# Kernel optimization log

Measured on AMD Instinct MI355X. Metric: run time of the kernel, lower is better.

The kernel has to match this reference:

```python
import jax, jax.numpy as jnp
import numpy as np

FRAME_LENGTH = 800
FRAME_STEP = 200
FFT_LENGTH = 800


def _hann_window(n):
    # tf.signal.hann_window default: periodic=True -> 0.5 - 0.5*cos(2*pi*k/n)
    k = jnp.arange(n, dtype=jnp.float32)
    return 0.5 - 0.5 * jnp.cos(2.0 * np.pi * k / n)


def setup_inputs() -> dict:
    key = jax.random.key(0)
    signals = jax.random.normal(key, (16, 240000), dtype=jnp.float32)
    window = _hann_window(FRAME_LENGTH)  # fft_length == frame_length, no pad
    n = jnp.arange(FFT_LENGTH, dtype=jnp.float32)
    angles = -2.0 * np.pi * n[:, None] * n[None, :] / float(FFT_LENGTH)  # [k, n]
    dft_cos = jnp.cos(angles)
    dft_sin = jnp.sin(angles)
    return {"signals": signals, "window": window, "dft_cos": dft_cos, "dft_sin": dft_sin}


def reference(signals, window, dft_cos, dft_sin):
    # Frame the signal: [B, num_frames, frame_length] via gather (pad_end=False)
    signal_length = signals.shape[1]
    num_frames = (signal_length - FRAME_LENGTH) // FRAME_STEP + 1
    starts = jnp.arange(num_frames, dtype=jnp.int32) * FRAME_STEP
    offsets = jnp.arange(FRAME_LENGTH, dtype=jnp.int32)
    idx = starts[:, None] + offsets[None, :]          # [F, L]
    frames = signals[:, idx]                          # [B, F, L]
    windowed = frames * window[:FRAME_LENGTH]         # [B, F, L]
    # Dense real/imag DFT: out[b,f,k] = sum_n windowed[b,f,n] * dft[k,n]
    real = jnp.einsum('bfn,kn->bfk', windowed, dft_cos)
    imag = jnp.einsum('bfn,kn->bfk', windowed, dft_sin)
    bins = FFT_LENGTH // 2 + 1
    return jnp.stack([real[:, :, :bins], imag[:, :, :bins]], axis=-1)  # [B, F, bins, 2]
```

## Files before the change

### kernel.cpp

```cpp
#include <hip/hip_runtime.h>
#include <hip/hip_bf16.h>

#define NBATCH   16
#define SIGLEN   240000
#define FRAMES   1197
#define M_TOTAL  (NBATCH * FRAMES)
#define K_TOTAL  800
#define NBINS    401
#define NOUT     (2 * NBINS)
#define FSTEP    200

#define KPAD  832
#define NTK   26
#define GBN   64
#define GMB   1024
#define GNT   13
#define GMT   19
#define GNWG  (GNT * GMT)
#define BSTR  840
#define NRG   1197

#define SIG_ELEMS  ((size_t)NBATCH * SIGLEN)
#define B_WS_ELEMS ((size_t)(GNT * GBN) * KPAD)
#define APK_ELEMS  ((size_t)NRG * NTK * 64 * 8)
#define WS_TIER2   ((SIG_ELEMS + B_WS_ELEMS) * 2)
#define WS_TIER1   ((SIG_ELEMS + B_WS_ELEMS + APK_ELEMS) * 2)

#define PREP_SIG_BLOCKS 1875
#define PREP_B_BLOCKS   338
#define PACK_TOTAL (NRG * NTK * 64)
#define PACK_BLOCKS ((PACK_TOTAL + 255) / 256)

typedef float  f32x4  __attribute__((ext_vector_type(4)));
typedef __bf16 bf16x8 __attribute__((ext_vector_type(8)));

static __device__ __forceinline__ unsigned f2bf_pair(float lo, float hi) {
    union { float f; unsigned u; } a, b;
    a.f = lo; b.f = hi;
    unsigned ua = (a.u + 0x7fffu + ((a.u >> 16) & 1u)) >> 16;
    unsigned ub = (b.u + 0x7fffu + ((b.u >> 16) & 1u)) >> 16;
    return ua | (ub << 16);
}

__global__ __launch_bounds__(256) void prep_all(
    const float* __restrict__ sig, const float* __restrict__ wnd,
    const float* __restrict__ dcos, const float* __restrict__ dsin,
    ushort* __restrict__ sbf, ushort* __restrict__ B)
{
    const int blk = blockIdx.x;
    if (blk < PREP_SIG_BLOCKS) {
        size_t i8 = ((size_t)blk * 256 + threadIdx.x) * 8;
        const float4 s0 = *(const float4*)(sig + i8);
        const float4 s1 = *(const float4*)(sig + i8 + 4);
        uint4 p;
        p.x = f2bf_pair(s0.x, s0.y);
        p.y = f2bf_pair(s0.z, s0.w);
        p.z = f2bf_pair(s1.x, s1.y);
        p.w = f2bf_pair(s1.z, s1.w);
        *(uint4*)(sbf + i8) = p;
    } else {
        int idx = (blk - PREP_SIG_BLOCKS) * 256 + threadIdx.x;
        int j  = idx / 104;
        int c8 = (idx - j * 104) * 8;
        uint4 p;
        if (j < NOUT && c8 < K_TOTAL) {
            const float* src = ((j & 1) ? dsin : dcos) + (size_t)(j >> 1) * K_TOTAL + c8;
            const float4 s0 = *(const float4*)(src);
            const float4 s1 = *(const float4*)(src + 4);
            const float4 w0 = *(const float4*)(wnd + c8);
            const float4 w1 = *(const float4*)(wnd + c8 + 4);
            p.x = f2bf_pair(s0.x * w0.x, s0.y * w0.y);
            p.y = f2bf_pair(s0.z * w0.z, s0.w * w0.w);
            p.z = f2bf_pair(s1.x * w1.x, s1.y * w1.y);
            p.w = f2bf_pair(s1.z * w1.z, s1.w * w1.w);
        } else {
            p = make_uint4(0u, 0u, 0u, 0u);
        }
        *(uint4*)(B + (size_t)j * KPAD + c8) = p;
    }
}

__global__ __launch_bounds__(256) void prep_pack(
    const ushort* __restrict__ sbf, ushort* __restrict__ Apk)
{
    int idx = blockIdx.x * 256 + threadIdx.x;
    if (idx >= PACK_TOTAL) return;
    const int lane   = idx & 63;
    const int kk     = (idx >> 6) % NTK;
    const int rowgrp = idx / (64 * NTK);
    const int row = rowgrp * 16 + (lane & 15);
    const int bb  = row / FRAMES, ff = row - bb * FRAMES;
    const ushort* src = sbf + (size_t)bb * SIGLEN + ff * FSTEP + kk * 32 + (lane >> 4) * 8;
    *(uint4*)(Apk + (size_t)idx * 8) = *(const uint4*)src;
}

__global__ __launch_bounds__(512, 2) void stft_gemm_pk(
    const ushort* __restrict__ Apk, const ushort* __restrict__ Bw,
    float* __restrict__ out)
{
    __shared__ ushort Bs[GBN * BSTR];

    const int tid  = threadIdx.x;

    const int orig = blockIdx.x;
    const int xcd  = orig & 7;
    const int idx  = orig >> 3;
    const int lbid = (xcd < 7 ? xcd * 31 : 217 + (xcd - 7) * 30) + idx;

    const int ntile = lbid % GNT;
    const int mblk  = lbid / GNT;
    const int j0    = ntile * GBN;
    const int m0    = mblk * GMB;

    const int wave = tid >> 6;
    const int lane = tid & 63;
    const int lr   = lane & 15;
    const int lg   = lane >> 4;
    const int mrow = m0 + wave * 128;

    const int g0 = (m0 >> 4) + wave * 8;
    size_t aBase[8];
    #pragma unroll
    for (int i = 0; i < 8; ++i) {
        int g = g0 + i;
        if (g >= NRG) g = NRG - 1;
        aBase[i] = (size_t)g * (NTK * 512) + lane * 8;
    }

    f32x4 acc[8][4];
    #pragma unroll
    for (int i = 0; i < 8; ++i)
        #pragma unroll
        for (int jj = 0; jj < 4; ++jj)
            acc[i][jj] = (f32x4){0.f, 0.f, 0.f, 0.f};

#define LOADA(A_, step) do {                                        \
        _Pragma("unroll")                                           \
        for (int i = 0; i < 8; ++i)                                 \
            A_[i] = *(const bf16x8*)(Apk + aBase[i] + (step) * 512);\
    } while (0)

#define LOADB(B_, step) do {                                        \
        const int kofs_ = (step) * 32;                              \
        _Pragma("unroll")                                           \
        for (int jj = 0; jj < 4; ++jj)                              \
            B_[jj] = *(const bf16x8*)&Bs[jj * (16 * BSTR) + lr * BSTR + lg * 8 + kofs_]; \
    } while (0)

#define MM(A_, B_) do {                                             \
        __builtin_amdgcn_s_setprio(1);                              \
        _Pragma("unroll")                                           \
        for (int i = 0; i < 8; ++i)                                 \
            _Pragma("unroll")                                       \
            for (int jj = 0; jj < 4; ++jj)                          \
                acc[i][jj] = __builtin_amdgcn_mfma_f32_16x16x32_bf16( \
                    A_[i], B_[jj], acc[i][jj], 0, 0, 0);            \
        __builtin_amdgcn_s_setprio(0);                              \
    } while (0)

    bf16x8 aX[8], aY[8], bX[4], bY[4];

    LOADA(aX, 0);
    LOADA(aY, 1);

    #pragma unroll
    for (int it = 0; it < 13; ++it) {
        int c   = tid + 512 * it;
        int row = c / 104;
        int col = (c - row * 104) * 8;
        *(uint4*)&Bs[row * BSTR + col] =
            *(const uint4*)(Bw + (size_t)(j0 + row) * KPAD + col);
    }
    __syncthreads();

    LOADB(bX, 0);
    LOADB(bY, 1);

    #pragma unroll 1
    for (int t = 0; t < NTK - 2; t += 2) {
        MM(aX, bX);
        LOADA(aX, t + 2);
        LOADB(bX, t + 2);
        MM(aY, bY);
        LOADA(aY, t + 3);
        LOADB(bY, t + 3);
    }
    MM(aX, bX);
    MM(aY, bY);

#undef LOADA
#undef LOADB
#undef MM

    #pragma unroll
    for (int i = 0; i < 8; ++i) {
        #pragma unroll
        for (int jj = 0; jj < 4; ++jj) {
            int col = j0 + jj * 16 + lr;
            if (col >= NOUT) continue;
            #pragma unroll
            for (int r = 0; r < 4; ++r) {
                int row = mrow + i * 16 + lg * 4 + r;
                if (row < M_TOTAL)
                    out[(size_t)row * NOUT + col] = acc[i][jj][r];
            }
        }
    }
}

__global__ __launch_bounds__(1024, 4) void stft_gemm_bp5(
    const ushort* __restrict__ sigbf, const ushort* __restrict__ Bw,
    float* __restrict__ out)
{
    __shared__ ushort Bs[GBN * BSTR];

    const int tid  = threadIdx.x;
    const int orig = blockIdx.x;
    const int xcd  = orig & 7;
    const int idx  = orig >> 3;
    const int lbid = (xcd < 7 ? xcd * 31 : 217 + (xcd - 7) * 30) + idx;

    const int ntile = lbid % GNT;
    const int mblk  = lbid / GNT;
    const int j0    = ntile * GBN;
    const int m0    = mblk * GMB;

    const int wave = tid >> 6;
    const int lane = tid & 63;
    const int lr   = lane & 15;
    const int lg   = lane >> 4;
    const int mrow = m0 + wave * 64;

    unsigned aOfs[4];
    #pragma unroll
    for (int i = 0; i < 4; ++i) {
        int row = mrow + i * 16 + lr;
        if (row >= M_TOTAL) row = M_TOTAL - 1;
        int bb = row / FRAMES, ff = row - bb * FRAMES;
        aOfs[i] = (unsigned)(bb * SIGLEN + ff * FSTEP + lg * 8);
    }
    const int bBase = lr * BSTR + lg * 8;

    f32x4 acc[4][4];
    #pragma unroll
    for (int i = 0; i < 4; ++i)
        #pragma unroll
        for (int jj = 0; jj < 4; ++jj)
            acc[i][jj] = (f32x4){0.f, 0.f, 0.f, 0.f};

#define LOADA(A_, step) do {                                        \
        const int kofs_ = (step) * 32;                              \
        _Pragma("unroll")                                           \
        for (int i = 0; i < 4; ++i)                                 \
            A_[i] = *(const bf16x8*)(sigbf + aOfs[i] + kofs_);      \
    } while (0)

#define LOADB(B_, step) do {                                        \
        const int kofs_ = (step) * 32;                              \
        _Pragma("unroll")                                           \
        for (int jj = 0; jj < 4; ++jj)                              \
            B_[jj] = *(const bf16x8*)&Bs[jj * (16 * BSTR) + bBase + kofs_]; \
    } while (0)

#define MM(A_, B_) do {                                             \
        __builtin_amdgcn_s_setprio(1);                              \
        _Pragma("unroll")                                           \
        for (int i = 0; i < 4; ++i)                                 \
            _Pragma("unroll")                                       \
            for (int jj = 0; jj < 4; ++jj)                          \
                acc[i][jj] = __builtin_amdgcn_mfma_f32_16x16x32_bf16( \
                    A_[i], B_[jj], acc[i][jj], 0, 0, 0);            \
        __builtin_amdgcn_s_setprio(0);                              \
    } while (0)

    bf16x8 aX[4], aY[4], bX[4];

    LOADA(aX, 0);
    LOADA(aY, 1);

    #pragma unroll
    for (int it = 0; it < 6; ++it) {
        int c   = tid + 1024 * it;
        int row = c / 104;
        int col = (c - row * 104) * 8;
        *(uint4*)&Bs[row * BSTR + col] =
            *(const uint4*)(Bw + (size_t)(j0 + row) * KPAD + col);
    }
    if (tid < 512) {
        int c   = tid + 6144;
        int row = c / 104;
        int col = (c - row * 104) * 8;
        *(uint4*)&Bs[row * BSTR + col] =
            *(const uint4*)(Bw + (size_t)(j0 + row) * KPAD + col);
    }
    __syncthreads();

    #pragma unroll 1
    for (int t = 0; t < NTK - 2; t += 2) {
        LOADB(bX, t);
        MM(aX, bX);
        LOADA(aX, t + 2);
        LOADB(bX, t + 1);
        MM(aY, bX);
        LOADA(aY, t + 3);
    }
    LOADB(bX, 24); MM(aX, bX);
    LOADB(bX, 25); MM(aY, bX);

#undef LOADA
#undef LOADB
#undef MM

    #pragma unroll
    for (int i = 0; i < 4; ++i) {
        #pragma unroll
        for (int jj = 0; jj < 4; ++jj) {
            int col = j0 + jj * 16 + lr;
            if (col >= NOUT) continue;
            #pragma unroll
            for (int r = 0; r < 4; ++r) {
                int row = mrow + i * 16 + lg * 4 + r;
                if (row < M_TOTAL)
                    out[(size_t)row * NOUT + col] = acc[i][jj][r];
            }
        }
    }
}

#define BM 128
#define BN 128
#define BK 32
#define NTILES_N 7
#define NTILES_M 150
#define NWG (NTILES_M * NTILES_N)
#define LDSS 40
__global__ __launch_bounds__(256) void stft_gemm_fb(
    const float* __restrict__ sig, const float* __restrict__ wnd,
    const float* __restrict__ dcos, const float* __restrict__ dsin,
    float* __restrict__ out)
{
    __shared__ ushort As[BM * LDSS];
    __shared__ ushort Bs[BN * LDSS];
    __shared__ int rowBase[BM];

    const int tid = threadIdx.x;
    const int bid = blockIdx.x;
    const int mt  = bid / NTILES_N;
    const int nt  = bid - mt * NTILES_N;
    const int m0  = mt * BM;
    const int j0  = nt * BN;

    if (tid < BM) {
        int m = m0 + tid;
        int v = -1;
        if (m < M_TOTAL) {
            int b  = m / FRAMES;
            int fl = m - b * FRAMES;
            v = b * SIGLEN + fl * FSTEP;
        }
        rowBase[tid] = v;
    }

    const int rS = tid >> 1;
    const int hS = tid & 1;

    const float* bRow = nullptr;
    {
        int j = j0 + rS;
        if (j < NOUT) {
            const float* srcm = (j & 1) ? dsin : dcos;
            bRow = srcm + (size_t)(j >> 1) * K_TOTAL;
        }
    }

    const int lane = tid & 63;
    const int wave = tid >> 6;
    const int wm   = wave >> 1;
    const int wn   = wave & 1;
    const int lr   = lane & 15;
    const int lg   = lane >> 4;

    f32x4 acc[4][4];
    #pragma unroll
    for (int i = 0; i < 4; ++i)
        #pragma unroll
        for (int jj = 0; jj < 4; ++jj)
            acc[i][jj] = (f32x4){0.f, 0.f, 0.f, 0.f};

    __syncthreads();

    for (int k0 = 0; k0 < K_TOTAL; k0 += BK) {
        {
            int base = rowBase[rS];
            float4 f0, f1, f2, f3;
            if (base >= 0) {
                const float4* sp = (const float4*)(sig + base + k0 + hS * 16);
                f0 = sp[0]; f1 = sp[1]; f2 = sp[2]; f3 = sp[3];
            } else {
                f0 = make_float4(0.f,0.f,0.f,0.f); f1 = f0; f2 = f0; f3 = f0;
            }
            const float4* wp = (const float4*)(wnd + k0 + hS * 16);
            float4 w0 = wp[0], w1 = wp[1], w2 = wp[2], w3 = wp[3];
            uint4 p0, p1;
            p0.x = f2bf_pair(f0.x * w0.x, f0.y * w0.y);
            p0.y = f2bf_pair(f0.z * w0.z, f0.w * w0.w);
            p0.z = f2bf_pair(f1.x * w1.x, f1.y * w1.y);
            p0.w = f2bf_pair(f1.z * w1.z, f1.w * w1.w);
            p1.x = f2bf_pair(f2.x * w2.x, f2.y * w2.y);
            p1.y = f2bf_pair(f2.z * w2.z, f2.w * w2.w);
            p1.z = f2bf_pair(f3.x * w3.x, f3.y * w3.y);
            p1.w = f2bf_pair(f3.z * w3.z, f3.w * w3.w);
            uint4* dst = (uint4*)&As[rS * LDSS + hS * 16];
            dst[0] = p0; dst[1] = p1;
        }
        {
            uint4 p0, p1;
            if (bRow) {
                const float4* sp = (const float4*)(bRow + k0 + hS * 16);
                float4 f0 = sp[0], f1 = sp[1], f2 = sp[2], f3 = sp[3];
                p0.x = f2bf_pair(f0.x, f0.y);
                p0.y = f2bf_pair(f0.z, f0.w);
                p0.z = f2bf_pair(f1.x, f1.y);
                p0.w = f2bf_pair(f1.z, f1.w);
                p1.x = f2bf_pair(f2.x, f2.y);
                p1.y = f2bf_pair(f2.z, f2.w);
                p1.z = f2bf_pair(f3.x, f3.y);
                p1.w = f2bf_pair(f3.z, f3.w);
            } else {
                p0 = make_uint4(0u,0u,0u,0u); p1 = p0;
            }
            uint4* dst = (uint4*)&Bs[rS * LDSS + hS * 16];
            dst[0] = p0; dst[1] = p1;
        }
        __syncthreads();

        bf16x8 a[4], b[4];
        #pragma unroll
        for (int i = 0; i < 4; ++i)
            a[i] = *(const bf16x8*)&As[(wm * 64 + i * 16 + lr) * LDSS + lg * 8];
        #pragma unroll
        for (int i = 0; i < 4; ++i)
            b[i] = *(const bf16x8*)&Bs[(wn * 64 + i * 16 + lr) * LDSS + lg * 8];
        #pragma unroll
        for (int i = 0; i < 4; ++i)
            #pragma unroll
            for (int jj = 0; jj < 4; ++jj)
                acc[i][jj] = __builtin_amdgcn_mfma_f32_16x16x32_bf16(a[i], b[jj], acc[i][jj], 0, 0, 0);

        __syncthreads();
    }

    const int mb = m0 + wm * 64;
    const int jb = j0 + wn * 64;
    #pragma unroll
    for (int i = 0; i < 4; ++i) {
        #pragma unroll
        for (int jj = 0; jj < 4; ++jj) {
            int col = jb + jj * 16 + lr;
            if (col >= NOUT) continue;
            #pragma unroll
            for (int r = 0; r < 4; ++r) {
                int row = mb + i * 16 + lg * 4 + r;
                if (row < M_TOTAL)
                    out[(size_t)row * NOUT + col] = acc[i][jj][r];
            }
        }
    }
}

extern "C" void kernel_launch(void* const* d_in, const int* in_sizes, int n_in,
                              void* d_out, int out_size, void* d_ws, size_t ws_size,
                              hipStream_t stream) {
    const float* sig  = (const float*)d_in[0];
    const float* wnd  = (const float*)d_in[1];
    const float* dcos = (const float*)d_in[2];
    const float* dsin = (const float*)d_in[3];
    float* out = (float*)d_out;

    if (ws_size >= WS_TIER1 && d_ws != nullptr) {
        ushort* sbf = (ushort*)d_ws;
        ushort* Bws = sbf + SIG_ELEMS;
        ushort* Apk = Bws + B_WS_ELEMS;
        prep_all<<<dim3(PREP_SIG_BLOCKS + PREP_B_BLOCKS), dim3(256), 0, stream>>>(
            sig, wnd, dcos, dsin, sbf, Bws);
        prep_pack<<<dim3(PACK_BLOCKS), dim3(256), 0, stream>>>(sbf, Apk);
        stft_gemm_pk<<<dim3(GNWG), dim3(512), 0, stream>>>(Apk, Bws, out);
    } else if (ws_size >= WS_TIER2 && d_ws != nullptr) {
        ushort* sbf = (ushort*)d_ws;
        ushort* Bws = sbf + SIG_ELEMS;
        prep_all<<<dim3(PREP_SIG_BLOCKS + PREP_B_BLOCKS), dim3(256), 0, stream>>>(
            sig, wnd, dcos, dsin, sbf, Bws);
        stft_gemm_bp5<<<dim3(GNWG), dim3(1024), 0, stream>>>(sbf, Bws, out);
    } else {
        stft_gemm_fb<<<dim3(NWG), dim3(256), 0, stream>>>(sig, wnd, dcos, dsin, out);
    }
}
```

Before: 63.72 us.

## Pack A directly from fp32 signal and coalesce GEMM output via LDS staging

The intermediate bf16 signal buffer is removed: prep_pack now reads the fp32 signal and converts it while packing, and a separate prep_b kernel builds the windowed DFT matrix. This cuts one full read-and-write pass over the signal, and the smaller workspace requirement makes the packed path eligible more often. The GEMM epilogue now stages each 16x64 accumulator tile in shared memory, then writes float4 rows instead of scattered scalar stores, improving write coalescing at the cost of extra LDS traffic and waits. The A offsets use 32-bit indices to reduce address arithmetic.

```diff
diff --git a/kernel.cpp b/kernel.cpp
--- a/kernel.cpp
+++ b/kernel.cpp
@@ -19,15 +19,16 @@
 #define GNWG  (GNT * GMT)
 #define BSTR  840
 #define NRG   1197
+#define SCSTR 68
 
 #define SIG_ELEMS  ((size_t)NBATCH * SIGLEN)
 #define B_WS_ELEMS ((size_t)(GNT * GBN) * KPAD)
 #define APK_ELEMS  ((size_t)NRG * NTK * 64 * 8)
+#define WS_TIER1   ((APK_ELEMS + B_WS_ELEMS) * 2)
 #define WS_TIER2   ((SIG_ELEMS + B_WS_ELEMS) * 2)
-#define WS_TIER1   ((SIG_ELEMS + B_WS_ELEMS + APK_ELEMS) * 2)
-
+
+#define PREP_B_BLOCKS 338
 #define PREP_SIG_BLOCKS 1875
-#define PREP_B_BLOCKS   338
 #define PACK_TOTAL (NRG * NTK * 64)
 #define PACK_BLOCKS ((PACK_TOTAL + 255) / 256)
 
@@ -40,6 +41,186 @@
     unsigned ua = (a.u + 0x7fffu + ((a.u >> 16) & 1u)) >> 16;
     unsigned ub = (b.u + 0x7fffu + ((b.u >> 16) & 1u)) >> 16;
     return ua | (ub << 16);
+}
+
+__global__ __launch_bounds__(256) void prep_b(
+    const float* __restrict__ dcos, const float* __restrict__ dsin,
+    const float* __restrict__ wnd, ushort* __restrict__ B)
+{
+    int idx = blockIdx.x * 256 + threadIdx.x;
+    int j  = idx / 104;
+    int c8 = (idx - j * 104) * 8;
+    uint4 p;
+    if (j < NOUT && c8 < K_TOTAL) {
+        const float* src = ((j & 1) ? dsin : dcos) + (size_t)(j >> 1) * K_TOTAL + c8;
+        const float4 s0 = *(const float4*)(src);
+        const float4 s1 = *(const float4*)(src + 4);
+        const float4 w0 = *(const float4*)(wnd + c8);
+        const float4 w1 = *(const float4*)(wnd + c8 + 4);
+        p.x = f2bf_pair(s0.x * w0.x, s0.y * w0.y);
+        p.y = f2bf_pair(s0.z * w0.z, s0.w * w0.w);
+        p.z = f2bf_pair(s1.x * w1.x, s1.y * w1.y);
+        p.w = f2bf_pair(s1.z * w1.z, s1.w * w1.w);
+    } else {
+        p = make_uint4(0u, 0u, 0u, 0u);
+    }
+    *(uint4*)(B + (size_t)j * KPAD + c8) = p;
+}
+
+__global__ __launch_bounds__(256) void prep_pack(
+    const float* __restrict__ sig, ushort* __restrict__ Apk)
+{
+    int idx = blockIdx.x * 256 + threadIdx.x;
+    if (idx >= PACK_TOTAL) return;
+    const int lane   = idx & 63;
+    const int kk     = (idx >> 6) % NTK;
+    const int rowgrp = idx / (64 * NTK);
+    const int row = rowgrp * 16 + (lane & 15);
+    const int bb  = row / FRAMES, ff = row - bb * FRAMES;
+    size_t off = (size_t)bb * SIGLEN + ff * FSTEP + kk * 32 + (lane >> 4) * 8;
+    if (off > SIG_ELEMS - 8) off = SIG_ELEMS - 8;
+    const float4 s0 = *(const float4*)(sig + off);
+    const float4 s1 = *(const float4*)(sig + off + 4);
+    uint4 p;
+    p.x = f2bf_pair(s0.x, s0.y);
+    p.y = f2bf_pair(s0.z, s0.w);
+    p.z = f2bf_pair(s1.x, s1.y);
+    p.w = f2bf_pair(s1.z, s1.w);
+    *(uint4*)(Apk + (size_t)idx * 8) = p;
+}
+
+__global__ __launch_bounds__(512, 2) void stft_gemm_pk(
+    const ushort* __restrict__ Apk, const ushort* __restrict__ Bw,
+    float* __restrict__ out)
+{
+    __shared__ ushort Bs[GBN * BSTR];
+
+    const int tid  = threadIdx.x;
+
+    const int orig = blockIdx.x;
+    const int xcd  = orig & 7;
+    const int idx  = orig >> 3;
+    const int lbid = (xcd < 7 ? xcd * 31 : 217 + (xcd - 7) * 30) + idx;
+
+    const int ntile = lbid % GNT;
+    const int mblk  = lbid / GNT;
+    const int j0    = ntile * GBN;
+    const int m0    = mblk * GMB;
+
+    const int wave = tid >> 6;
+    const int lane = tid & 63;
+    const int lr   = lane & 15;
+    const int lg   = lane >> 4;
+    const int mrow = m0 + wave * 128;
+
+    const int g0 = (m0 >> 4) + wave * 8;
+    unsigned aBase[8];
+    #pragma unroll
+    for (int i = 0; i < 8; ++i) {
+        int g = g0 + i;
+        if (g >= NRG) g = NRG - 1;
+        aBase[i] = (unsigned)g * (NTK * 512) + lane * 8;
+    }
+
+    f32x4 acc[8][4];
+    #pragma unroll
+    for (int i = 0; i < 8; ++i)
+        #pragma unroll
+        for (int jj = 0; jj < 4; ++jj)
+            acc[i][jj] = (f32x4){0.f, 0.f, 0.f, 0.f};
+
+#define LOADA(A_, step) do {                                        \
+        _Pragma("unroll")                                           \
+        for (int i = 0; i < 8; ++i)                                 \
+            A_[i] = *(const bf16x8*)(Apk + (size_t)aBase[i] + (step) * 512); \
+    } while (0)
+
+#define LOADB(B_, step) do {                                        \
+        const int kofs_ = (step) * 32;                              \
+        _Pragma("unroll")                                           \
+        for (int jj = 0; jj < 4; ++jj)                              \
+            B_[jj] = *(const bf16x8*)&Bs[jj * (16 * BSTR) + lr * BSTR + lg * 8 + kofs_]; \
+    } while (0)
+
+#define MM(A_, B_) do {                                             \
+        __builtin_amdgcn_s_setprio(1);                              \
+        _Pragma("unroll")                                           \
+        for (int i = 0; i < 8; ++i)                                 \
+            _Pragma("unroll")                                       \
+            for (int jj = 0; jj < 4; ++jj)                          \
+                acc[i][jj] = __builtin_amdgcn_mfma_f32_16x16x32_bf16( \
+                    A_[i], B_[jj], acc[i][jj], 0, 0, 0);            \
+        __builtin_amdgcn_s_setprio(0);                              \
+    } while (0)
+
+    bf16x8 aX[8], aY[8], bX[4], bY[4];
+
+    LOADA(aX, 0);
+    LOADA(aY, 1);
+
+    #pragma unroll
+    for (int it = 0; it < 13; ++it) {
+        int c   = tid + 512 * it;
+        int row = c / 104;
+        int col = (c - row * 104) * 8;
+        *(uint4*)&Bs[row * BSTR + col] =
+            *(const uint4*)(Bw + (size_t)(j0 + row) * KPAD + col);
+    }
+    __syncthreads();
+
+    LOADB(bX, 0);
+    LOADB(bY, 1);
+
+    #pragma unroll 1
+    for (int t = 0; t < NTK - 2; t += 2) {
+        MM(aX, bX);
+        LOADA(aX, t + 2);
+        LOADB(bX, t + 2);
+        MM(aY, bY);
+        LOADA(aY, t + 3);
+        LOADB(bY, t + 3);
+    }
+    MM(aX, bX);
+    MM(aY, bY);
+
+#undef LOADA
+#undef LOADB
+#undef MM
+
+    __syncthreads();
+    float* sc = (float*)Bs + wave * (16 * SCSTR);
+    const int rl = lane >> 2;
+    const int kq = lane & 3;
+
+    #pragma unroll
+    for (int i = 0; i < 8; ++i) {
+        __builtin_amdgcn_sched_barrier(0);
+        #pragma unroll
+        for (int jj = 0; jj < 4; ++jj)
+            #pragma unroll
+            for (int r = 0; r < 4; ++r)
+                sc[(lg * 4 + r) * SCSTR + jj * 16 + lr] = acc[i][jj][r];
+        asm volatile("s_waitcnt lgkmcnt(0)" ::: "memory");
+        __builtin_amdgcn_sched_barrier(0);
+        int row = mrow + i * 16 + rl;
+        if (row < M_TOTAL) {
+            float* op = out + (size_t)row * NOUT;
+            #pragma unroll
+            for (int ch = 0; ch < 4; ++ch) {
+                int colb = j0 + ch * 16 + kq * 4;
+                float4 v = *(float4*)&sc[rl * SCSTR + ch * 16 + kq * 4];
+                if (colb + 3 < NOUT) {
+                    *(float4*)(op + colb) = v;
+                } else {
+                    #pragma unroll
+                    for (int e = 0; e < 4; ++e)
+                        if (colb + e < NOUT) op[colb + e] = ((float*)&v)[e];
+                }
+            }
+        }
+        asm volatile("s_waitcnt lgkmcnt(0)" ::: "memory");
+        __builtin_amdgcn_sched_barrier(0);
+    }
 }
 
 __global__ __launch_bounds__(256) void prep_all(
@@ -80,134 +261,6 @@
     }
 }
 
-__global__ __launch_bounds__(256) void prep_pack(
-    const ushort* __restrict__ sbf, ushort* __restrict__ Apk)
-{
-    int idx = blockIdx.x * 256 + threadIdx.x;
-    if (idx >= PACK_TOTAL) return;
-    const int lane   = idx & 63;
-    const int kk     = (idx >> 6) % NTK;
-    const int rowgrp = idx / (64 * NTK);
-    const int row = rowgrp * 16 + (lane & 15);
-    const int bb  = row / FRAMES, ff = row - bb * FRAMES;
-    const ushort* src = sbf + (size_t)bb * SIGLEN + ff * FSTEP + kk * 32 + (lane >> 4) * 8;
-    *(uint4*)(Apk + (size_t)idx * 8) = *(const uint4*)src;
-}
-
-__global__ __launch_bounds__(512, 2) void stft_gemm_pk(
-    const ushort* __restrict__ Apk, const ushort* __restrict__ Bw,
-    float* __restrict__ out)
-{
-    __shared__ ushort Bs[GBN * BSTR];
-
-    const int tid  = threadIdx.x;
-
-    const int orig = blockIdx.x;
-    const int xcd  = orig & 7;
-    const int idx  = orig >> 3;
-    const int lbid = (xcd < 7 ? xcd * 31 : 217 + (xcd - 7) * 30) + idx;
-
-    const int ntile = lbid % GNT;
-    const int mblk  = lbid / GNT;
-    const int j0    = ntile * GBN;
-    const int m0    = mblk * GMB;
-
-    const int wave = tid >> 6;
-    const int lane = tid & 63;
-    const int lr   = lane & 15;
-    const int lg   = lane >> 4;
-    const int mrow = m0 + wave * 128;
-
-    const int g0 = (m0 >> 4) + wave * 8;
-    size_t aBase[8];
-    #pragma unroll
-    for (int i = 0; i < 8; ++i) {
-        int g = g0 + i;
-        if (g >= NRG) g = NRG - 1;
-        aBase[i] = (size_t)g * (NTK * 512) + lane * 8;
-    }
-
-    f32x4 acc[8][4];
-    #pragma unroll
-    for (int i = 0; i < 8; ++i)
-        #pragma unroll
-        for (int jj = 0; jj < 4; ++jj)
-            acc[i][jj] = (f32x4){0.f, 0.f, 0.f, 0.f};
-
-#define LOADA(A_, step) do {                                        \
-        _Pragma("unroll")                                           \
-        for (int i = 0; i < 8; ++i)                                 \
-            A_[i] = *(const bf16x8*)(Apk + aBase[i] + (step) * 512);\
-    } while (0)
-
-#define LOADB(B_, step) do {                                        \
-        const int kofs_ = (step) * 32;                              \
-        _Pragma("unroll")                                           \
-        for (int jj = 0; jj < 4; ++jj)                              \
-            B_[jj] = *(const bf16x8*)&Bs[jj * (16 * BSTR) + lr * BSTR + lg * 8 + kofs_]; \
-    } while (0)
-
-#define MM(A_, B_) do {                                             \
-        __builtin_amdgcn_s_setprio(1);                              \
-        _Pragma("unroll")                                           \
-        for (int i = 0; i < 8; ++i)                                 \
-            _Pragma("unroll")                                       \
-            for (int jj = 0; jj < 4; ++jj)                          \
-                acc[i][jj] = __builtin_amdgcn_mfma_f32_16x16x32_bf16( \
-                    A_[i], B_[jj], acc[i][jj], 0, 0, 0);            \
-        __builtin_amdgcn_s_setprio(0);                              \
-    } while (0)
-
-    bf16x8 aX[8], aY[8], bX[4], bY[4];
-
-    LOADA(aX, 0);
-    LOADA(aY, 1);
-
-    #pragma unroll
-    for (int it = 0; it < 13; ++it) {
-        int c   = tid + 512 * it;
-        int row = c / 104;
-        int col = (c - row * 104) * 8;
-        *(uint4*)&Bs[row * BSTR + col] =
-            *(const uint4*)(Bw + (size_t)(j0 + row) * KPAD + col);
-    }
-    __syncthreads();
-
-    LOADB(bX, 0);
-    LOADB(bY, 1);
-
-    #pragma unroll 1
-    for (int t = 0; t < NTK - 2; t += 2) {
-        MM(aX, bX);
-        LOADA(aX, t + 2);
-        LOADB(bX, t + 2);
-        MM(aY, bY);
-        LOADA(aY, t + 3);
-        LOADB(bY, t + 3);
-    }
-    MM(aX, bX);
-    MM(aY, bY);
-
-#undef LOADA
-#undef LOADB
-#undef MM
-
-    #pragma unroll
-    for (int i = 0; i < 8; ++i) {
-        #pragma unroll
-        for (int jj = 0; jj < 4; ++jj) {
-            int col = j0 + jj * 16 + lr;
-            if (col >= NOUT) continue;
-            #pragma unroll
-            for (int r = 0; r < 4; ++r) {
-                int row = mrow + i * 16 + lg * 4 + r;
-                if (row < M_TOTAL)
-                    out[(size_t)row * NOUT + col] = acc[i][jj][r];
-            }
-        }
-    }
-}
-
 __global__ __launch_bounds__(1024, 4) void stft_gemm_bp5(
     const ushort* __restrict__ sigbf, const ushort* __restrict__ Bw,
     float* __restrict__ out)
@@ -478,12 +531,10 @@
     float* out = (float*)d_out;
 
     if (ws_size >= WS_TIER1 && d_ws != nullptr) {
-        ushort* sbf = (ushort*)d_ws;
-        ushort* Bws = sbf + SIG_ELEMS;
-        ushort* Apk = Bws + B_WS_ELEMS;
-        prep_all<<<dim3(PREP_SIG_BLOCKS + PREP_B_BLOCKS), dim3(256), 0, stream>>>(
-            sig, wnd, dcos, dsin, sbf, Bws);
-        prep_pack<<<dim3(PACK_BLOCKS), dim3(256), 0, stream>>>(sbf, Apk);
+        ushort* Apk = (ushort*)d_ws;
+        ushort* Bws = Apk + APK_ELEMS;
+        prep_b<<<dim3(PREP_B_BLOCKS), dim3(256), 0, stream>>>(dcos, dsin, wnd, Bws);
+        prep_pack<<<dim3(PACK_BLOCKS), dim3(256), 0, stream>>>(sig, Apk);
         stft_gemm_pk<<<dim3(GNWG), dim3(512), 0, stream>>>(Apk, Bws, out);
     } else if (ws_size >= WS_TIER2 && d_ws != nullptr) {
         ushort* sbf = (ushort*)d_ws;
```

Result: faster. 61.24 us (-3.9%).
